# Optimization experiments

Hardware: AMD Instinct MI355X
Metric: run time of the kernel (lower is better)

Reference implementation:

```python
import jax
import jax.numpy as jnp
import numpy as np
from jax import lax

DELTA = float(np.exp(-2.0))  # rule-creation density threshold


def codebook_lamb(x):
    """Online growing RBF prototype codebook (ALMMo-style) for one layer.

    x: [N, M]. Returns lamb: [N] normalized density of each sample at its
    assigned rule. Faithful (corrected) semantics of Layer.__call__:
      - SEN = squared L2 norm per sample (over feature dim)
      - global mean / mean squared norm over the batch
      - sequential per-sample: if max RBF density over existing rules < exp(-2),
        append a new rule (prototype=c=x, SENc=||x||^2, support=1);
        else update rule_star. Note the source's `support[rule_star] = +1`
        assigns 1, so the running mean update degenerates to c[rule_star]=x,
        SENc[rule_star]=||x||^2 -- replicated here.
      - distances use the (never-updated) prototypes; bandwidth stau uses c.
    """
    N, M = x.shape
    SENx = jnp.sum(x * x, axis=-1)                      # [N]
    gmean = jnp.mean(x, axis=0)                         # [M]
    base = jnp.mean(SENx) - jnp.sum(gmean * gmean)      # SENgmean - SEN(gmean)
    R = N                                               # worst case: one rule/sample

    protos0 = jnp.zeros((R, M), x.dtype)
    pn20 = jnp.zeros((R,), x.dtype)                     # ||proto_r||^2 (carried)
    c0 = jnp.zeros((R, M), x.dtype)
    cn20 = jnp.zeros((R,), x.dtype)                     # ||c_r||^2 (carried)
    SENc0 = jnp.zeros((R,), x.dtype)
    count0 = jnp.int32(0)

    ridx = jnp.arange(R)

    def step(carry, inp):
        protos, pn2, c, cn2, SENc, count = carry
        xi, sxi = inp                                   # [M], scalar
        valid = ridx < count
        stau = (base + SENc - cn2) * 0.5                # [R]
        dist = sxi + pn2 - 2.0 * (protos @ xi)          # [R] ||xi - proto_r||^2
        dens = jnp.where(valid, jnp.exp(-dist / stau), -jnp.inf)
        idx = jnp.argmax(dens)
        vmax = dens[idx]
        new = (count == 0) | (vmax < DELTA)
        slot = jnp.where(new, count, idx)
        # both branches set c/SENc at slot to xi/sxi (support resets to 1)
        c = c.at[slot].set(xi)
        cn2 = cn2.at[slot].set(sxi)
        SENc = SENc.at[slot].set(sxi)
        # only a new rule writes a prototype (OOB scatter when count==R is dropped)
        protos = protos.at[count].set(jnp.where(new, xi, protos[count]))
        pn2 = pn2.at[count].set(jnp.where(new, sxi, pn2[count]))
        count = count + new.astype(count.dtype)
        return (protos, pn2, c, cn2, SENc, count), slot

    (protos, pn2, c, cn2, SENc, count), rules = lax.scan(
        step, (protos0, pn20, c0, cn20, SENc0, count0), (x, SENx)
    )

    # final densities of all samples under all (valid) rules: [R, N]
    stau = (base + SENc - cn2) * 0.5                    # [R]
    dist = SENx[None, :] + pn2[:, None] - 2.0 * (protos @ x.T)
    dens = jnp.where((ridx < count)[:, None], jnp.exp(-dist / stau[:, None]), 0.0)
    dens_xn = dens[rules, jnp.arange(N)]                # density at assigned rule
    lamb = dens_xn / jnp.sum(dens, axis=0)              # normalize over rules
    return lamb


def setup_inputs() -> dict:
    key = jax.random.key(0)
    k = jax.random.split(key, 5)
    N, D_IN, D_H, D_OUT = 2048, 2048, 2048, 1024
    s0 = 1.0 / np.sqrt(D_IN)
    s1 = 1.0 / np.sqrt(D_H)
    return {
        "x": jax.random.normal(k[0], (N, D_IN), jnp.float32),
        "W0": jax.random.normal(k[1], (D_H, D_IN), jnp.float32) * s0,
        "b0": jax.random.normal(k[2], (D_H,), jnp.float32) * s0,
        "W1": jax.random.normal(k[3], (D_OUT, D_H), jnp.float32) * s1,
        "b1": jax.random.normal(k[4], (D_OUT,), jnp.float32) * s1,
    }


def reference(x, W0, b0, W1, b1):
    lambs = []
    h = x
    for W, b in ((W0, b0), (W1, b1)):
        lambs.append(codebook_lamb(h))          # per-layer codebook on layer input
        h = jax.nn.sigmoid(h @ W.T + b)         # torch.nn.Linear + sigmoid
    return h, jnp.stack(lambs)                  # ([N, d_out], [n_layers, N])
```

## Files before the change

kernel.cpp:

```cpp
#include <hip/hip_runtime.h>
#include <cstdint>
#include <cstddef>


#define DELTA_F 0.13533528323661270f
#define MBYTE (1u << 20)
#define ZRE_WORDS 16400

typedef __bf16 bf16;
typedef bf16 bf16x8 __attribute__((ext_vector_type(8)));
typedef bf16 bf16x4 __attribute__((ext_vector_type(4)));
typedef float f32x4 __attribute__((ext_vector_type(4)));

typedef __attribute__((address_space(1))) void as1_void;
typedef __attribute__((address_space(3))) void as3_void;

__device__ __forceinline__ void gload16(const bf16* g, bf16* l) {
  __builtin_amdgcn_global_load_lds((as1_void*)g, (as3_void*)l, 16, 0, 0);
}

__device__ __forceinline__ float wave_reduce(float s) {
  for (int o = 32; o > 0; o >>= 1) s += __shfl_down(s, o, 64);
  return s;
}

template <bool IS_L0>
__global__ __launch_bounds__(512, 4) void gemm_fused(
    const bf16* __restrict__ A, float* __restrict__ Dens,
    bf16* __restrict__ Hb, float* __restrict__ Fo,
    const float* __restrict__ bias, const float* __restrict__ SENin,
    const float* __restrict__ ninv_p, float* __restrict__ S,
    int* __restrict__ e, float* __restrict__ SENhOut,
    float* __restrict__ colsumH, float* __restrict__ diagD,
    int* __restrict__ cnt, float* __restrict__ scalOut,
    float* __restrict__ lambOut, int nblocks) {
  __shared__ __align__(16) char smem[32768];
  __shared__ int s_last;
  const int tid = threadIdx.x;
  const int wave = tid >> 6, lane = tid & 63;
  const int quad = lane >> 4, l16 = lane & 15;
  const int kg = wave & 1, wm = (wave >> 1) & 1, wn = (wave >> 2) & 1;
  const int m0 = blockIdx.y * 128, n0 = blockIdx.x * 128;
  const int waveM = wm * 64, waveN = wn * 64;
  const bool isGram = (n0 < 2048);
  const int sr8 = lane >> 3, slot = lane & 7;
  const int gk = (slot ^ sr8) * 8;
  const bf16* aSrc = A + (size_t)(m0 + wave * 16 + sr8) * 2048 + gk;
  const bf16* bSrc = A + (size_t)(n0 + wave * 16 + sr8) * 2048 + gk;
  char* const aDst = smem + wave * 2048;
  char* const bDst = smem + 16384 + wave * 2048;
  const int swz = ((kg * 4 + quad) ^ (l16 & 7)) * 16;
  const int aOff = (waveM + l16) * 128 + swz;
  const int bOff = 16384 + (waveN + l16) * 128 + swz;

  f32x4 acc[4][4] = {};
  for (int k0 = 0; k0 < 2048; k0 += 64) {
    gload16(aSrc + k0, (bf16*)aDst);
    gload16(aSrc + 8 * 2048 + k0, (bf16*)(aDst + 1024));
    gload16(bSrc + k0, (bf16*)bDst);
    gload16(bSrc + 8 * 2048 + k0, (bf16*)(bDst + 1024));
    __syncthreads();
    bf16x8 af[4], bfr[4];
#pragma unroll
    for (int i = 0; i < 4; ++i) af[i] = *(const bf16x8*)(smem + aOff + i * 2048);
#pragma unroll
    for (int j = 0; j < 4; ++j) bfr[j] = *(const bf16x8*)(smem + bOff + j * 2048);
#pragma unroll
    for (int i = 0; i < 4; ++i)
#pragma unroll
      for (int j = 0; j < 4; ++j)
        acc[i][j] = __builtin_amdgcn_mfma_f32_16x16x32_bf16(af[i], bfr[j], acc[i][j], 0, 0, 0);
    __syncthreads();
  }

  const float ninv = ninv_p[0];
  float colp[4] = {0.f, 0.f, 0.f, 0.f};
  char* const ex = smem + (wn * 2 + wm) * 8192;
#pragma unroll
  for (int round = 0; round < 2; ++round) {
    __syncthreads();
    if (kg == 1) {
#pragma unroll
      for (int ii = 0; ii < 2; ++ii)
#pragma unroll
        for (int j = 0; j < 4; ++j)
          *(f32x4*)(ex + (ii * 4 + j) * 1024 + lane * 16) = acc[round * 2 + ii][j];
    }
    __syncthreads();
    if (kg == 0) {
#pragma unroll
      for (int ii = 0; ii < 2; ++ii) {
        const int i = round * 2 + ii;
        const int rbase = m0 + waveM + i * 16 + quad * 4;
        if (isGram) {
          const f32x4 si4 = *(const f32x4*)(SENin + rbase);
          float rp[4] = {0.f, 0.f, 0.f, 0.f};
          int er = 0;
#pragma unroll
          for (int j = 0; j < 4; ++j) {
            f32x4 v = acc[i][j] + *(const f32x4*)(ex + (ii * 4 + j) * 1024 + lane * 16);
            const int col = n0 + waveN + j * 16 + l16;
            const float sj = SENin[col];
#pragma unroll
            for (int r = 0; r < 4; ++r) {
              const float dens = __expf((si4[r] + sj - 2.0f * v[r]) * ninv);
              Dens[(size_t)(rbase + r) * 2048 + col] = dens;
              rp[r] += dens;
              if (col < rbase + r && dens >= DELTA_F) er |= (1 << r);
              if (col == rbase + r) atomicExch(diagD + col, dens);
            }
          }
#pragma unroll
          for (int r = 0; r < 4; ++r) {
            float rv = rp[r];
            rv += __shfl_xor(rv, 1, 64); rv += __shfl_xor(rv, 2, 64);
            rv += __shfl_xor(rv, 4, 64); rv += __shfl_xor(rv, 8, 64);
            if (l16 == 0) atomicAdd(S + rbase + r, rv);
          }
          er |= __shfl_xor(er, 1, 64); er |= __shfl_xor(er, 2, 64);
          er |= __shfl_xor(er, 4, 64); er |= __shfl_xor(er, 8, 64);
          if (l16 == 0 && er) {
#pragma unroll
            for (int r = 0; r < 4; ++r)
              if ((er >> r) & 1) atomicOr(e + rbase + r, 1);
          }
        } else {
          float rn[4] = {0.f, 0.f, 0.f, 0.f};
#pragma unroll
          for (int j = 0; j < 4; ++j) {
            f32x4 v = acc[i][j] + *(const f32x4*)(ex + (ii * 4 + j) * 1024 + lane * 16);
            const int c2 = n0 - 2048 + waveN + j * 16 + l16;
            const float bv = bias[c2];
#pragma unroll
            for (int r = 0; r < 4; ++r) {
              const float hv = 1.0f / (1.0f + __expf(-(v[r] + bv)));
              if (IS_L0) {
                Hb[(size_t)(rbase + r) * 2048 + c2] = (bf16)hv;
                rn[r] += hv * hv;
                colp[j] += hv;
              } else {
                Fo[(size_t)(rbase + r) * 1024 + c2] = hv;
              }
            }
          }
          if (IS_L0) {
#pragma unroll
            for (int r = 0; r < 4; ++r) {
              float rv = rn[r];
              rv += __shfl_xor(rv, 1, 64); rv += __shfl_xor(rv, 2, 64);
              rv += __shfl_xor(rv, 4, 64); rv += __shfl_xor(rv, 8, 64);
              if (l16 == 0) atomicAdd(SENhOut + rbase + r, rv);
            }
          }
        }
      }
    }
  }
  if (IS_L0 && !isGram && kg == 0) {
#pragma unroll
    for (int j = 0; j < 4; ++j) {
      float cv = colp[j];
      cv += __shfl_xor(cv, 16, 64);
      cv += __shfl_xor(cv, 32, 64);
      if (lane < 16) atomicAdd(colsumH + (n0 - 2048 + waveN + j * 16 + lane), cv);
    }
  }

  __syncthreads();
  if (tid == 0) {
    __threadfence();
    s_last = (atomicAdd(cnt, 1) == nblocks - 1);
  }
  __syncthreads();
  if (!s_last) return;
  __threadfence();

  char* s_flag = smem;
  short* s_as = (short*)(smem + 2048);
  short* s_list = (short*)(smem + 6144);
  short* s_re = (short*)(smem + 10240);
  int* scan_ = (int*)(smem + 14336);
  float* rbest = (float*)(smem + 16384);
  int* rbj = (int*)(smem + 18432);
  float* r1 = (float*)(smem + 20480);
  float* r2 = (float*)(smem + 22528);
  int* sT = (int*)(smem + 24576);
  int* sReN = (int*)(smem + 24580);

  if (IS_L0) {
    float ssen = 0.f, sg2 = 0.f;
    for (int i = tid; i < 2048; i += 512) ssen += atomicAdd(SENhOut + i, 0.f);
    for (int c = tid; c < 2048; c += 512) {
      const float gm = atomicAdd(colsumH + c, 0.f) * (1.f / 2048.f);
      sg2 += gm * gm;
    }
    r1[tid] = ssen; r2[tid] = sg2;
    __syncthreads();
    for (int s = 256; s; s >>= 1) {
      if (tid < s) { r1[tid] += r1[tid + s]; r2[tid] += r2[tid + s]; }
      __syncthreads();
    }
    if (tid == 0) {
      const float stau = 0.5f * (r1[0] * (1.f / 2048.f) - r2[0]);
      scalOut[4] = stau;
      scalOut[5] = -1.f / stau;
    }
    __syncthreads();
  }

  int cntl = 0;
#pragma unroll
  for (int k = 0; k < 4; ++k) {
    const int i = tid * 4 + k;
    const int ei = atomicOr(e + i, 0);
    s_flag[i] = (ei == 0);
    if (ei == 0) s_as[i] = (short)i;
    cntl += (ei != 0);
  }
  scan_[tid] = cntl;
  if (tid == 0) sReN[0] = 0;
  __syncthreads();
  for (int off = 1; off < 512; off <<= 1) {
    const int v = scan_[tid];
    const int add = (tid >= off) ? scan_[tid - off] : 0;
    __syncthreads();
    scan_[tid] = v + add;
    __syncthreads();
  }
  int pos = scan_[tid] - cntl;
#pragma unroll
  for (int k = 0; k < 4; ++k) {
    const int i = tid * 4 + k;
    if (!s_flag[i]) s_list[pos++] = (short)i;
  }
  if (tid == 511) sT[0] = scan_[511];
  __syncthreads();
  const int T = sT[0];
  for (int t = 0; t < T; ++t) {
    const int i = s_list[t];
    const float* di = Dens + (size_t)i * 2048;
    float best = -1.0f;
    int bestj = 0x7fffffff;
    for (int j = tid; j < i; j += 512) {
      if (s_flag[j]) {
        const float d = di[j];
        if (d > best || (d == best && j < bestj)) { best = d; bestj = j; }
      }
    }
    rbest[tid] = best; rbj[tid] = bestj;
    __syncthreads();
    if (tid == 0) {
      float b = -1.0f;
      int bj = 0x7fffffff;
      for (int k = 0; k < 512; ++k)
        if (rbest[k] > b || (rbest[k] == b && rbj[k] < bj)) { b = rbest[k]; bj = rbj[k]; }
      if (b < DELTA_F) { s_flag[i] = 1; s_as[i] = (short)i; }
      else { s_as[i] = (short)bj; s_re[sReN[0]++] = (short)i; }
    }
    __syncthreads();
  }
  const int reN = sReN[0];

#pragma unroll
  for (int k = 0; k < 4; ++k) {
    const int n = k * 512 + tid;
    const int aa = s_as[n];
    const float num = (aa == n) ? atomicAdd(diagD + n, 0.f)
                                : Dens[(size_t)n * 2048 + aa];
    float denom = atomicAdd(S + n, 0.f);
    for (int t = 0; t < reN; ++t) denom -= Dens[(size_t)n * 2048 + s_re[t]];
    lambOut[n] = num / denom;
  }
}

__global__ void f2b_all(const float* __restrict__ x, const float* __restrict__ W0,
                        const float* __restrict__ W1, bf16* __restrict__ xb,
                        bf16* __restrict__ wb0, bf16* __restrict__ wb1,
                        float* __restrict__ SENx, float* __restrict__ cpart,
                        int* __restrict__ zre) {
  const int b = blockIdx.x, tid = threadIdx.x;
  const int wave = tid >> 6, lane = tid & 63;
  if (b < 256) {
    const int r0 = b * 8;
    __shared__ float ws[8][4];
    f32x4 c0 = {0.f, 0.f, 0.f, 0.f}, c1 = {0.f, 0.f, 0.f, 0.f};
    for (int r = 0; r < 8; ++r) {
      const float* src = x + (size_t)(r0 + r) * 2048;
      bf16* dst = xb + (size_t)(r0 + r) * 2048;
      f32x4 v0 = *(const f32x4*)(src + tid * 4);
      f32x4 v1 = *(const f32x4*)(src + 1024 + tid * 4);
      bf16x4 o0, o1;
      o0.x = (bf16)v0.x; o0.y = (bf16)v0.y; o0.z = (bf16)v0.z; o0.w = (bf16)v0.w;
      o1.x = (bf16)v1.x; o1.y = (bf16)v1.y; o1.z = (bf16)v1.z; o1.w = (bf16)v1.w;
      *(bf16x4*)(dst + tid * 4) = o0;
      *(bf16x4*)(dst + 1024 + tid * 4) = o1;
      c0 += v0; c1 += v1;
      float rn = v0.x * v0.x + v0.y * v0.y + v0.z * v0.z + v0.w * v0.w +
                 v1.x * v1.x + v1.y * v1.y + v1.z * v1.z + v1.w * v1.w;
      rn = wave_reduce(rn);
      if (lane == 0) ws[r][wave] = rn;
    }
    __syncthreads();
    if (tid < 8) SENx[r0 + tid] = ws[tid][0] + ws[tid][1] + ws[tid][2] + ws[tid][3];
    float* bin = cpart + (size_t)b * 2048;
    *(f32x4*)(bin + tid * 4) = c0;
    *(f32x4*)(bin + 1024 + tid * 4) = c1;
  } else if (b < 512) {
    const size_t base = (size_t)(b - 256) * 16384;
    for (int c = tid * 4; c < 16384; c += 1024) {
      f32x4 v = *(const f32x4*)(W0 + base + c);
      bf16x4 o;
      o.x = (bf16)v.x; o.y = (bf16)v.y; o.z = (bf16)v.z; o.w = (bf16)v.w;
      *(bf16x4*)(wb0 + base + c) = o;
    }
  } else {
    const size_t base = (size_t)(b - 512) * 16384;
    for (int c = tid * 4; c < 16384; c += 1024) {
      f32x4 v = *(const f32x4*)(W1 + base + c);
      bf16x4 o;
      o.x = (bf16)v.x; o.y = (bf16)v.y; o.z = (bf16)v.z; o.w = (bf16)v.w;
      *(bf16x4*)(wb1 + base + c) = o;
    }
    const int idx = (b - 512) * 256 + tid;
    if (idx < ZRE_WORDS) zre[idx] = 0;
  }
}

__global__ void stau0_kernel(const float* __restrict__ SENx,
                             const float* __restrict__ cpart,
                             float* __restrict__ accS, float* __restrict__ accG,
                             int* __restrict__ cntS, float* __restrict__ scal) {
  const int p = blockIdx.x, tid = threadIdx.x;
  const int col = p * 256 + tid;
  float s = 0.f;
  for (int r = 0; r < 256; ++r) s += cpart[(size_t)r * 2048 + col];
  const float gm = s * (1.f / 2048.f);
  float sg2 = gm * gm;
  float ssen = 0.f;
  if (p == 0)
    for (int i = tid; i < 2048; i += 256) ssen += SENx[i];
  __shared__ float r1[256], r2[256];
  __shared__ int s_last;
  r1[tid] = sg2; r2[tid] = ssen;
  __syncthreads();
  for (int st = 128; st; st >>= 1) {
    if (tid < st) { r1[tid] += r1[tid + st]; r2[tid] += r2[tid + st]; }
    __syncthreads();
  }
  if (tid == 0) {
    atomicAdd(accG, r1[0]);
    if (p == 0) atomicAdd(accS, r2[0]);
    __threadfence();
    s_last = (atomicAdd(cntS, 1) == 7);
  }
  __syncthreads();
  if (tid == 0 && s_last) {
    const float vG = atomicAdd(accG, 0.f);
    const float vS = atomicAdd(accS, 0.f);
    const float stau = 0.5f * (vS * (1.f / 2048.f) - vG);
    scal[0] = stau;
    scal[1] = -1.f / stau;
  }
}

extern "C" void kernel_launch(void* const* d_in, const int* in_sizes, int n_in,
                              void* d_out, int out_size, void* d_ws, size_t ws_size,
                              hipStream_t stream) {
  const float* x = (const float*)d_in[0];
  const float* W0 = (const float*)d_in[1];
  const float* b0 = (const float*)d_in[2];
  const float* W1 = (const float*)d_in[3];
  const float* b1 = (const float*)d_in[4];
  float* out = (float*)d_out;

  char* w = (char*)d_ws;
  bf16* xb = (bf16*)(w);
  bf16* wb0 = (bf16*)(w + 8 * MBYTE);
  bf16* hb = (bf16*)(w + 16 * MBYTE);
  bf16* wb1 = (bf16*)(w + 24 * MBYTE);
  float* Dens = (float*)(w + 28 * MBYTE);
  float* SENx = (float*)(w + 44 * MBYTE);
  float* cpart = SENx + 2048;
  float* scal = cpart + 256 * 2048;
  float* zre = scal + 16;
  float* SENh = zre;
  float* colsumH = SENh + 2048;
  float* S0 = colsumH + 2048;
  float* S1 = S0 + 2048;
  float* diagD0 = S1 + 2048;
  float* diagD1 = diagD0 + 2048;
  int* e0 = (int*)(diagD1 + 2048);
  int* e1 = e0 + 2048;
  float* accS = (float*)(e1 + 2048);
  float* accG = accS + 1;
  int* cntS = (int*)(accG + 1);
  int* cnt0 = cntS + 1;
  int* cnt1 = cnt0 + 1;

  float* lamb0 = out + (size_t)2048 * 1024;
  float* lamb1 = lamb0 + 2048;

  f2b_all<<<640, 256, 0, stream>>>(x, W0, W1, xb, wb0, wb1, SENx, cpart, (int*)zre);
  stau0_kernel<<<8, 256, 0, stream>>>(SENx, cpart, accS, accG, cntS, scal);
  gemm_fused<true><<<dim3(32, 16), 512, 0, stream>>>(
      xb, Dens, hb, nullptr, b0, SENx, scal + 1, S0, e0, SENh, colsumH,
      diagD0, cnt0, scal, lamb0, 512);
  gemm_fused<false><<<dim3(24, 16), 512, 0, stream>>>(
      hb, Dens, nullptr, out, b1, SENh, scal + 5, S1, e1, nullptr, nullptr,
      diagD1, cnt1, nullptr, lamb1, 384);
}
```

Before: 229.9 us.

## Fold stau reduction into conversion kernel via last-block pattern and atomic bins

Removes the separate stau0 kernel launch. The conversion kernel now atomically accumulates column sums into 16 bins and lets the last finishing block compute stau. Zeroing of the accumulators moves to a hipMemsetAsync. The threadfence in the GEMM's last-block path becomes conditional, running only when the sequential rule scan has work. Risks include atomic contention on the bins, the extra cost of the memset, and weaker memory ordering from dropping the fences.

After: 203.4 us. -11.5%, faster.

```diff
diff --git a/kernel.cpp b/kernel.cpp
--- a/kernel.cpp
+++ b/kernel.cpp
@@ -5,7 +5,6 @@
 
 #define DELTA_F 0.13533528323661270f
 #define MBYTE (1u << 20)
-#define ZRE_WORDS 16400
 
 typedef __bf16 bf16;
 typedef bf16 bf16x8 __attribute__((ext_vector_type(8)));
@@ -167,13 +166,9 @@
   }
 
   __syncthreads();
-  if (tid == 0) {
-    __threadfence();
-    s_last = (atomicAdd(cnt, 1) == nblocks - 1);
-  }
+  if (tid == 0) s_last = (atomicAdd(cnt, 1) == nblocks - 1);
   __syncthreads();
   if (!s_last) return;
-  __threadfence();
 
   char* s_flag = smem;
   short* s_as = (short*)(smem + 2048);
@@ -236,6 +231,7 @@
   if (tid == 511) sT[0] = scan_[511];
   __syncthreads();
   const int T = sT[0];
+  if (T > 0) __threadfence();
   for (int t = 0; t < T; ++t) {
     const int i = s_list[t];
     const float* di = Dens + (size_t)i * 2048;
@@ -276,13 +272,15 @@
 __global__ void f2b_all(const float* __restrict__ x, const float* __restrict__ W0,
                         const float* __restrict__ W1, bf16* __restrict__ xb,
                         bf16* __restrict__ wb0, bf16* __restrict__ wb1,
-                        float* __restrict__ SENx, float* __restrict__ cpart,
-                        int* __restrict__ zre) {
+                        float* __restrict__ SENx, float* __restrict__ bins,
+                        int* __restrict__ cntF, float* __restrict__ scal) {
   const int b = blockIdx.x, tid = threadIdx.x;
   const int wave = tid >> 6, lane = tid & 63;
+  __shared__ float ws[8][4];
+  __shared__ float red1[256], red2[256];
+  __shared__ int s_last;
   if (b < 256) {
     const int r0 = b * 8;
-    __shared__ float ws[8][4];
     f32x4 c0 = {0.f, 0.f, 0.f, 0.f}, c1 = {0.f, 0.f, 0.f, 0.f};
     for (int r = 0; r < 8; ++r) {
       const float* src = x + (size_t)(r0 + r) * 2048;
@@ -301,10 +299,13 @@
       if (lane == 0) ws[r][wave] = rn;
     }
     __syncthreads();
-    if (tid < 8) SENx[r0 + tid] = ws[tid][0] + ws[tid][1] + ws[tid][2] + ws[tid][3];
-    float* bin = cpart + (size_t)b * 2048;
-    *(f32x4*)(bin + tid * 4) = c0;
-    *(f32x4*)(bin + 1024 + tid * 4) = c1;
+    if (tid < 8)
+      atomicExch(SENx + r0 + tid, ws[tid][0] + ws[tid][1] + ws[tid][2] + ws[tid][3]);
+    float* bin = bins + (size_t)(b & 15) * 2048;
+    atomicAdd(bin + tid * 4 + 0, c0.x); atomicAdd(bin + tid * 4 + 1, c0.y);
+    atomicAdd(bin + tid * 4 + 2, c0.z); atomicAdd(bin + tid * 4 + 3, c0.w);
+    atomicAdd(bin + 1024 + tid * 4 + 0, c1.x); atomicAdd(bin + 1024 + tid * 4 + 1, c1.y);
+    atomicAdd(bin + 1024 + tid * 4 + 2, c1.z); atomicAdd(bin + 1024 + tid * 4 + 3, c1.w);
   } else if (b < 512) {
     const size_t base = (size_t)(b - 256) * 16384;
     for (int c = tid * 4; c < 16384; c += 1024) {
@@ -321,43 +322,30 @@
       o.x = (bf16)v.x; o.y = (bf16)v.y; o.z = (bf16)v.z; o.w = (bf16)v.w;
       *(bf16x4*)(wb1 + base + c) = o;
     }
-    const int idx = (b - 512) * 256 + tid;
-    if (idx < ZRE_WORDS) zre[idx] = 0;
-  }
-}
-
-__global__ void stau0_kernel(const float* __restrict__ SENx,
-                             const float* __restrict__ cpart,
-                             float* __restrict__ accS, float* __restrict__ accG,
-                             int* __restrict__ cntS, float* __restrict__ scal) {
-  const int p = blockIdx.x, tid = threadIdx.x;
-  const int col = p * 256 + tid;
-  float s = 0.f;
-  for (int r = 0; r < 256; ++r) s += cpart[(size_t)r * 2048 + col];
-  const float gm = s * (1.f / 2048.f);
-  float sg2 = gm * gm;
+  }
+
+  __syncthreads();
+  if (tid == 0) s_last = (atomicAdd(cntF, 1) == 639);
+  __syncthreads();
+  if (!s_last) return;
   float ssen = 0.f;
-  if (p == 0)
-    for (int i = tid; i < 2048; i += 256) ssen += SENx[i];
-  __shared__ float r1[256], r2[256];
-  __shared__ int s_last;
-  r1[tid] = sg2; r2[tid] = ssen;
-  __syncthreads();
-  for (int st = 128; st; st >>= 1) {
-    if (tid < st) { r1[tid] += r1[tid + st]; r2[tid] += r2[tid + st]; }
+  for (int i = tid; i < 2048; i += 256) ssen += atomicAdd(SENx + i, 0.f);
+  float sg2 = 0.f;
+  for (int c = tid; c < 2048; c += 256) {
+    float cs = 0.f;
+#pragma unroll
+    for (int p = 0; p < 16; ++p) cs += atomicAdd(bins + (size_t)p * 2048 + c, 0.f);
+    const float gm = cs * (1.f / 2048.f);
+    sg2 += gm * gm;
+  }
+  red1[tid] = ssen; red2[tid] = sg2;
+  __syncthreads();
+  for (int s = 128; s; s >>= 1) {
+    if (tid < s) { red1[tid] += red1[tid + s]; red2[tid] += red2[tid + s]; }
     __syncthreads();
   }
   if (tid == 0) {
-    atomicAdd(accG, r1[0]);
-    if (p == 0) atomicAdd(accS, r2[0]);
-    __threadfence();
-    s_last = (atomicAdd(cntS, 1) == 7);
-  }
-  __syncthreads();
-  if (tid == 0 && s_last) {
-    const float vG = atomicAdd(accG, 0.f);
-    const float vS = atomicAdd(accS, 0.f);
-    const float stau = 0.5f * (vS * (1.f / 2048.f) - vG);
+    const float stau = 0.5f * (red1[0] * (1.f / 2048.f) - red2[0]);
     scal[0] = stau;
     scal[1] = -1.f / stau;
   }
@@ -380,10 +368,10 @@
   bf16* wb1 = (bf16*)(w + 24 * MBYTE);
   float* Dens = (float*)(w + 28 * MBYTE);
   float* SENx = (float*)(w + 44 * MBYTE);
-  float* cpart = SENx + 2048;
-  float* scal = cpart + 256 * 2048;
+  float* scal = SENx + 2048;
   float* zre = scal + 16;
-  float* SENh = zre;
+  float* bins = zre;
+  float* SENh = bins + 16 * 2048;
   float* colsumH = SENh + 2048;
   float* S0 = colsumH + 2048;
   float* S1 = S0 + 2048;
@@ -391,17 +379,16 @@
   float* diagD1 = diagD0 + 2048;
   int* e0 = (int*)(diagD1 + 2048);
   int* e1 = e0 + 2048;
-  float* accS = (float*)(e1 + 2048);
-  float* accG = accS + 1;
-  int* cntS = (int*)(accG + 1);
-  int* cnt0 = cntS + 1;
+  int* cntF = e1 + 2048;
+  int* cnt0 = cntF + 1;
   int* cnt1 = cnt0 + 1;
+  const size_t zwords = 16 * 2048 + 8 * 2048 + 16;
 
   float* lamb0 = out + (size_t)2048 * 1024;
   float* lamb1 = lamb0 + 2048;
 
-  f2b_all<<<640, 256, 0, stream>>>(x, W0, W1, xb, wb0, wb1, SENx, cpart, (int*)zre);
-  stau0_kernel<<<8, 256, 0, stream>>>(SENx, cpart, accS, accG, cntS, scal);
+  hipMemsetAsync(zre, 0, zwords * 4, stream);
+  f2b_all<<<640, 256, 0, stream>>>(x, W0, W1, xb, wb0, wb1, SENx, bins, cntF, scal);
   gemm_fused<true><<<dim3(32, 16), 512, 0, stream>>>(
       xb, Dens, hb, nullptr, b0, SENx, scal + 1, S0, e0, SENh, colsumH,
       diagD0, cnt0, scal, lamb0, 512);
```
